# Kernel tuning notes

Hardware: AMD Instinct MI355X
Metric: run time of the kernel (lower is better)

The kernel has to match this reference:

```python
import jax, jax.numpy as jnp
import numpy as np

D_MODEL, D_K, D_V = 1024, 64, 64
B, S = 4, 2048

def setup_inputs() -> dict:
    key = jax.random.key(0)
    ks = jax.random.split(key, 9)
    lim = 1.0 / np.sqrt(D_MODEL)
    return {
        "query": jax.random.normal(ks[0], (B, S, D_MODEL), jnp.float32),
        "key":   jax.random.normal(ks[1], (B, S, D_MODEL), jnp.float32),
        "value": jax.random.normal(ks[2], (B, S, D_MODEL), jnp.float32),
        "Wq": jax.random.uniform(ks[3], (D_MODEL, D_K), jnp.float32, -lim, lim),
        "bq": jax.random.uniform(ks[4], (D_K,), jnp.float32, -lim, lim),
        "Wk": jax.random.uniform(ks[5], (D_MODEL, D_K), jnp.float32, -lim, lim),
        "bk": jax.random.uniform(ks[6], (D_K,), jnp.float32, -lim, lim),
        "Wv": jax.random.uniform(ks[7], (D_MODEL, D_V), jnp.float32, -lim, lim),
        "bv": jax.random.uniform(ks[8], (D_V,), jnp.float32, -lim, lim),
    }

def reference(query, key, value, Wq, bq, Wk, bk, Wv, bv):
    # Linear projections: [B,S,d_model] -> [B,S,d_k/d_v]
    q = jnp.einsum("bsd,dk->bsk", query, Wq) + bq
    k = jnp.einsum("bsd,dk->bsk", key, Wk) + bk
    v = jnp.einsum("bsd,dv->bsv", value, Wv) + bv
    scale = 1.0 / jnp.sqrt(jnp.asarray(q.shape[-1], q.dtype))
    scores = jnp.einsum("bqk,bsk->bqs", q, k) * scale  # [B,S,S]
    attn = jax.nn.softmax(scores, axis=-1)
    return jnp.einsum("bqs,bsv->bqv", attn, v)  # [B,S,d_v]
```

## Files before the change

kernel.cpp:

```cpp
#include <hip/hip_runtime.h>
#include <hip/hip_bf16.h>


typedef __attribute__((ext_vector_type(8))) short bf16x8;
typedef __attribute__((ext_vector_type(4))) float f32x4;

#define MFMA16(a, b, c) __builtin_amdgcn_mfma_f32_16x16x32_bf16((a), (b), (c), 0, 0, 0)

__device__ __forceinline__ unsigned short f2bf(float x) {
    unsigned int u = __float_as_uint(x);
    u = (u + 0x7FFFu + ((u >> 16) & 1u)) >> 16;
    return (unsigned short)u;
}

__global__ __launch_bounds__(256) void prep_w(
    const float* __restrict__ Wq, const float* __restrict__ Wk,
    const float* __restrict__ Wv, unsigned short* __restrict__ Wt) {
    int idx = blockIdx.x * 256 + threadIdx.x;
    int t = idx >> 16;
    int r = idx & 0xFFFF;
    int n = r >> 10, kk = r & 1023;
    const float* W = (t == 0) ? Wq : ((t == 1) ? Wk : Wv);
    Wt[idx] = f2bf(W[kk * 64 + n]);
}

__global__ __launch_bounds__(256) void proj_kernel(
    const float* __restrict__ xq, const float* __restrict__ xk,
    const float* __restrict__ xv, const unsigned short* __restrict__ Wt,
    const float* __restrict__ bq, const float* __restrict__ bk,
    const float* __restrict__ bv, unsigned short* __restrict__ outq,
    unsigned short* __restrict__ outk, unsigned short* __restrict__ outvt) {
    const int chunk = blockIdx.x;
    const int t = chunk >> 8;
    const int rb = chunk & 255;
    const int row0 = rb * 32;
    const float* __restrict__ x = (t == 0) ? xq : ((t == 1) ? xk : xv);
    const float* __restrict__ bias = (t == 0) ? bq : ((t == 1) ? bk : bv);
    const unsigned short* __restrict__ Wtt = Wt + t * 65536;

    __shared__ __align__(16) unsigned short xl[32][72];
    __shared__ __align__(16) unsigned short wl[64][72];

    const int tid = threadIdx.x;
    const int w = tid >> 6, l = tid & 63;
    const int lo = l & 15, q4 = l >> 4;
    const int rowt = (w & 1) * 16;
    const int colb = (w >> 1) * 32;

    const int lr = tid >> 3;
    const int lkc = (tid & 7) * 8;
    const int wr = tid >> 2;
    const int wkc = (tid & 3) * 16;

    f32x4 acc[2];
    for (int i = 0; i < 2; i++)
        for (int j = 0; j < 4; j++) acc[i][j] = 0.f;

    const float* xrow = x + (size_t)(row0 + lr) * 1024 + lkc;
    const unsigned short* wrow = Wtt + (size_t)wr * 1024 + wkc;

    float4 px0 = *(const float4*)(xrow);
    float4 px1 = *(const float4*)(xrow + 4);
    int4 pw0 = *(const int4*)(wrow);
    int4 pw1 = *(const int4*)(wrow + 8);

    for (int s = 0; s < 16; ++s) {
        __syncthreads();
        {
            int4 d;
            d.x = f2bf(px0.x) | ((int)f2bf(px0.y) << 16);
            d.y = f2bf(px0.z) | ((int)f2bf(px0.w) << 16);
            d.z = f2bf(px1.x) | ((int)f2bf(px1.y) << 16);
            d.w = f2bf(px1.z) | ((int)f2bf(px1.w) << 16);
            *(int4*)&xl[lr][lkc] = d;
            *(int4*)&wl[wr][wkc] = pw0;
            *(int4*)&wl[wr][wkc + 8] = pw1;
        }
        __syncthreads();
        if (s < 15) {
            const float* xn = xrow + (s + 1) * 64;
            px0 = *(const float4*)(xn);
            px1 = *(const float4*)(xn + 4);
            const unsigned short* wn = wrow + (s + 1) * 64;
            pw0 = *(const int4*)(wn);
            pw1 = *(const int4*)(wn + 8);
        }
        bf16x8 a0 = *(const bf16x8*)&xl[rowt + lo][q4 * 8];
        bf16x8 a1 = *(const bf16x8*)&xl[rowt + lo][32 + q4 * 8];
#pragma unroll
        for (int ci = 0; ci < 2; ++ci) {
            bf16x8 b0 = *(const bf16x8*)&wl[colb + ci * 16 + lo][q4 * 8];
            bf16x8 b1 = *(const bf16x8*)&wl[colb + ci * 16 + lo][32 + q4 * 8];
            acc[ci] = MFMA16(a0, b0, acc[ci]);
            acc[ci] = MFMA16(a1, b1, acc[ci]);
        }
    }
#pragma unroll
    for (int ci = 0; ci < 2; ++ci) {
        float bb = bias[colb + ci * 16 + lo];
#pragma unroll
        for (int i = 0; i < 4; i++) acc[ci][i] += bb;
    }
    if (t == 0) {
        const float SC = 0.125f * 1.44269504088896340736f;
#pragma unroll
        for (int ci = 0; ci < 2; ++ci)
#pragma unroll
            for (int i = 0; i < 4; i++) acc[ci][i] *= SC;
    }
    if (t < 2) {
        unsigned short* out = (t == 0) ? outq : outk;
#pragma unroll
        for (int ci = 0; ci < 2; ++ci)
#pragma unroll
            for (int i = 0; i < 4; i++)
                out[(size_t)(row0 + rowt + q4 * 4 + i) * 64 + colb + ci * 16 + lo] =
                    f2bf(acc[ci][i]);
    } else {
        int b = row0 >> 11;
        int sl = (row0 & 2047) + rowt + q4 * 4;
#pragma unroll
        for (int ci = 0; ci < 2; ++ci) {
            int vf = colb + ci * 16 + lo;
            ushort4 h;
            h.x = f2bf(acc[ci][0]);
            h.y = f2bf(acc[ci][1]);
            h.z = f2bf(acc[ci][2]);
            h.w = f2bf(acc[ci][3]);
            *(ushort4*)&outvt[(size_t)(b * 64 + vf) * 2048 + sl] = h;
        }
    }
}

__global__ __launch_bounds__(256) void flash_kernel(
    const unsigned short* __restrict__ q, const unsigned short* __restrict__ k,
    const unsigned short* __restrict__ vt, float* __restrict__ Opart,
    float* __restrict__ lpart) {
    const int bx = blockIdx.x;
    const int xcd = bx & 7;
    const int b = xcd >> 1;
    const int j = ((bx >> 3) << 1) | (xcd & 1);
    const int ks = j & 3;
    const int qb = j >> 2;
    const int w = threadIdx.x >> 6, l = threadIdx.x & 63;
    const int lo = l & 15, q4 = l >> 4;

    __shared__ __align__(16) unsigned short pl[4][16][72];

    const int srow = qb * 64 + w * 16;

    const unsigned short* qp = q + (size_t)(b * 2048 + srow + lo) * 64 + q4 * 8;
    bf16x8 aq0 = *(const bf16x8*)(qp);
    bf16x8 aq1 = *(const bf16x8*)(qp + 32);

    f32x4 O[4];
    for (int i = 0; i < 4; i++)
        for (int j2 = 0; j2 < 4; j2++) O[i][j2] = 0.f;
    float ll[4] = {0.f, 0.f, 0.f, 0.f};

    for (int kt = 0; kt < 8; ++kt) {
        const int kb = ks * 512 + kt * 64;
        f32x4 S[4];
        for (int i = 0; i < 4; i++)
            for (int j2 = 0; j2 < 4; j2++) S[i][j2] = 0.f;
        const unsigned short* kp = k + (size_t)(b * 2048 + kb + lo) * 64 + q4 * 8;
#pragma unroll
        for (int ct = 0; ct < 4; ++ct) {
            bf16x8 b0 = *(const bf16x8*)(kp + ct * 1024);
            bf16x8 b1 = *(const bf16x8*)(kp + ct * 1024 + 32);
            S[ct] = MFMA16(aq0, b0, S[ct]);
            S[ct] = MFMA16(aq1, b1, S[ct]);
        }
#pragma unroll
        for (int i = 0; i < 4; i++) {
#pragma unroll
            for (int ct = 0; ct < 4; ++ct) {
                float p = exp2f(S[ct][i]);
                S[ct][i] = p;
                ll[i] += p;
            }
#pragma unroll
            for (int ct = 0; ct < 4; ++ct)
                pl[w][q4 * 4 + i][ct * 16 + lo] = f2bf(S[ct][i]);
        }
        bf16x8 ap0 = *(const bf16x8*)&pl[w][lo][q4 * 8];
        bf16x8 ap1 = *(const bf16x8*)&pl[w][lo][32 + q4 * 8];
        const unsigned short* vp =
            vt + (size_t)(b * 64 + lo) * 2048 + kb + q4 * 8;
#pragma unroll
        for (int ct = 0; ct < 4; ++ct) {
            bf16x8 v0 = *(const bf16x8*)(vp + (size_t)ct * 16 * 2048);
            bf16x8 v1 = *(const bf16x8*)(vp + (size_t)ct * 16 * 2048 + 32);
            O[ct] = MFMA16(ap0, v0, O[ct]);
            O[ct] = MFMA16(ap1, v1, O[ct]);
        }
    }
    float* op = Opart + ((size_t)(b * 4 + ks) * 2048 + srow) * 64;
#pragma unroll
    for (int ct = 0; ct < 4; ++ct)
#pragma unroll
        for (int i = 0; i < 4; i++)
            op[(size_t)(q4 * 4 + i) * 64 + ct * 16 + lo] = O[ct][i];
#pragma unroll
    for (int i = 0; i < 4; i++) {
        float s = ll[i];
        s += __shfl_xor(s, 1);
        s += __shfl_xor(s, 2);
        s += __shfl_xor(s, 4);
        s += __shfl_xor(s, 8);
        if (lo == 0)
            lpart[(size_t)(b * 4 + ks) * 2048 + srow + q4 * 4 + i] = s;
    }
}

__global__ __launch_bounds__(256) void combine_kernel(
    const float* __restrict__ Opart, const float* __restrict__ lpart,
    float* __restrict__ out) {
    int idx = blockIdx.x * 256 + threadIdx.x;
    int rowi = idx >> 4;
    int v4 = (idx & 15) * 4;
    int b = rowi >> 11, s = rowi & 2047;
    float L = 0.f;
#pragma unroll
    for (int ks = 0; ks < 4; ++ks)
        L += lpart[(size_t)(b * 4 + ks) * 2048 + s];
    float inv = 1.f / L;
    float ax = 0.f, ay = 0.f, az = 0.f, aw = 0.f;
#pragma unroll
    for (int ks = 0; ks < 4; ++ks) {
        const float4 o =
            *(const float4*)&Opart[((size_t)(b * 4 + ks) * 2048 + s) * 64 + v4];
        ax += o.x;
        ay += o.y;
        az += o.z;
        aw += o.w;
    }
    float4 res = make_float4(ax * inv, ay * inv, az * inv, aw * inv);
    *(float4*)&out[(size_t)rowi * 64 + v4] = res;
}

extern "C" void kernel_launch(void* const* d_in, const int* in_sizes, int n_in,
                              void* d_out, int out_size, void* d_ws,
                              size_t ws_size, hipStream_t stream) {
    const float* xq = (const float*)d_in[0];
    const float* xk = (const float*)d_in[1];
    const float* xv = (const float*)d_in[2];
    const float* Wq = (const float*)d_in[3];
    const float* bq = (const float*)d_in[4];
    const float* Wk = (const float*)d_in[5];
    const float* bk = (const float*)d_in[6];
    const float* Wv = (const float*)d_in[7];
    const float* bv = (const float*)d_in[8];
    float* out = (float*)d_out;

    char* ws = (char*)d_ws;
    unsigned short* qb = (unsigned short*)(ws);
    unsigned short* kb = (unsigned short*)(ws + (1u << 20));
    unsigned short* vtb = (unsigned short*)(ws + (2u << 20));
    unsigned short* Wt = (unsigned short*)(ws + (3u << 20));
    float* Opart = (float*)(ws + 3538944);
    float* lpart = (float*)(ws + 11927552);

    hipLaunchKernelGGL(prep_w, dim3(768), dim3(256), 0, stream, Wq, Wk, Wv, Wt);
    hipLaunchKernelGGL(proj_kernel, dim3(768), dim3(256), 0, stream, xq, xk, xv,
                       Wt, bq, bk, bv, qb, kb, vtb);
    hipLaunchKernelGGL(flash_kernel, dim3(512), dim3(256), 0, stream, qb, kb,
                       vtb, Opart, lpart);
    hipLaunchKernelGGL(combine_kernel, dim3(512), dim3(256), 0, stream, Opart,
                       lpart, out);
}
```

Baseline: 174.4 us.

## Load projection operands directly into MFMA registers, dropping LDS staging

The projection kernel no longer stages x and W tiles through shared memory with barriers. Each wave now loads its fp32 x fragment and bf16 W fragment straight from global memory into MFMA operand registers, with a 16-row tile per block and twice as many blocks. This removes the LDS round-trips and __syncthreads overhead. In exchange, the four waves of a block each re-read the same x rows from global memory or cache, and the 16-byte-per-lane loads are strided by row, which may coalesce less well.

After: 211.7 us. +21.4%, slower.

```diff
diff --git a/kernel.cpp b/kernel.cpp
--- a/kernel.cpp
+++ b/kernel.cpp
@@ -31,104 +31,61 @@
     const float* __restrict__ bv, unsigned short* __restrict__ outq,
     unsigned short* __restrict__ outk, unsigned short* __restrict__ outvt) {
     const int chunk = blockIdx.x;
-    const int t = chunk >> 8;
-    const int rb = chunk & 255;
-    const int row0 = rb * 32;
+    const int t = chunk >> 9;
+    const int rb = chunk & 511;
+    const int row0 = rb * 16;
     const float* __restrict__ x = (t == 0) ? xq : ((t == 1) ? xk : xv);
     const float* __restrict__ bias = (t == 0) ? bq : ((t == 1) ? bk : bv);
-    const unsigned short* __restrict__ Wtt = Wt + t * 65536;
-
-    __shared__ __align__(16) unsigned short xl[32][72];
-    __shared__ __align__(16) unsigned short wl[64][72];
 
     const int tid = threadIdx.x;
     const int w = tid >> 6, l = tid & 63;
     const int lo = l & 15, q4 = l >> 4;
-    const int rowt = (w & 1) * 16;
-    const int colb = (w >> 1) * 32;
-
-    const int lr = tid >> 3;
-    const int lkc = (tid & 7) * 8;
-    const int wr = tid >> 2;
-    const int wkc = (tid & 3) * 16;
-
-    f32x4 acc[2];
-    for (int i = 0; i < 2; i++)
-        for (int j = 0; j < 4; j++) acc[i][j] = 0.f;
-
-    const float* xrow = x + (size_t)(row0 + lr) * 1024 + lkc;
-    const unsigned short* wrow = Wtt + (size_t)wr * 1024 + wkc;
-
-    float4 px0 = *(const float4*)(xrow);
-    float4 px1 = *(const float4*)(xrow + 4);
-    int4 pw0 = *(const int4*)(wrow);
-    int4 pw1 = *(const int4*)(wrow + 8);
-
-    for (int s = 0; s < 16; ++s) {
-        __syncthreads();
-        {
-            int4 d;
-            d.x = f2bf(px0.x) | ((int)f2bf(px0.y) << 16);
-            d.y = f2bf(px0.z) | ((int)f2bf(px0.w) << 16);
-            d.z = f2bf(px1.x) | ((int)f2bf(px1.y) << 16);
-            d.w = f2bf(px1.z) | ((int)f2bf(px1.w) << 16);
-            *(int4*)&xl[lr][lkc] = d;
-            *(int4*)&wl[wr][wkc] = pw0;
-            *(int4*)&wl[wr][wkc + 8] = pw1;
-        }
-        __syncthreads();
-        if (s < 15) {
-            const float* xn = xrow + (s + 1) * 64;
-            px0 = *(const float4*)(xn);
-            px1 = *(const float4*)(xn + 4);
-            const unsigned short* wn = wrow + (s + 1) * 64;
-            pw0 = *(const int4*)(wn);
-            pw1 = *(const int4*)(wn + 8);
-        }
-        bf16x8 a0 = *(const bf16x8*)&xl[rowt + lo][q4 * 8];
-        bf16x8 a1 = *(const bf16x8*)&xl[rowt + lo][32 + q4 * 8];
-#pragma unroll
-        for (int ci = 0; ci < 2; ++ci) {
-            bf16x8 b0 = *(const bf16x8*)&wl[colb + ci * 16 + lo][q4 * 8];
-            bf16x8 b1 = *(const bf16x8*)&wl[colb + ci * 16 + lo][32 + q4 * 8];
-            acc[ci] = MFMA16(a0, b0, acc[ci]);
-            acc[ci] = MFMA16(a1, b1, acc[ci]);
-        }
-    }
-#pragma unroll
-    for (int ci = 0; ci < 2; ++ci) {
-        float bb = bias[colb + ci * 16 + lo];
-#pragma unroll
-        for (int i = 0; i < 4; i++) acc[ci][i] += bb;
-    }
+
+    const float* __restrict__ xrow = x + (size_t)(row0 + lo) * 1024 + q4 * 8;
+    const unsigned short* __restrict__ wrow =
+        Wt + (size_t)t * 65536 + (size_t)(w * 16 + lo) * 1024 + q4 * 8;
+
+    f32x4 acc = {0.f, 0.f, 0.f, 0.f};
+#pragma unroll 8
+    for (int kk = 0; kk < 32; ++kk) {
+        float4 xa = *(const float4*)(xrow + kk * 32);
+        float4 xb = *(const float4*)(xrow + kk * 32 + 4);
+        bf16x8 bw = *(const bf16x8*)(wrow + kk * 32);
+        bf16x8 av;
+        av[0] = (short)f2bf(xa.x);
+        av[1] = (short)f2bf(xa.y);
+        av[2] = (short)f2bf(xa.z);
+        av[3] = (short)f2bf(xa.w);
+        av[4] = (short)f2bf(xb.x);
+        av[5] = (short)f2bf(xb.y);
+        av[6] = (short)f2bf(xb.z);
+        av[7] = (short)f2bf(xb.w);
+        acc = MFMA16(av, bw, acc);
+    }
+
+    float bb = bias[w * 16 + lo];
+#pragma unroll
+    for (int i = 0; i < 4; i++) acc[i] += bb;
     if (t == 0) {
         const float SC = 0.125f * 1.44269504088896340736f;
 #pragma unroll
-        for (int ci = 0; ci < 2; ++ci)
-#pragma unroll
-            for (int i = 0; i < 4; i++) acc[ci][i] *= SC;
+        for (int i = 0; i < 4; i++) acc[i] *= SC;
     }
     if (t < 2) {
         unsigned short* out = (t == 0) ? outq : outk;
 #pragma unroll
-        for (int ci = 0; ci < 2; ++ci)
-#pragma unroll
-            for (int i = 0; i < 4; i++)
-                out[(size_t)(row0 + rowt + q4 * 4 + i) * 64 + colb + ci * 16 + lo] =
-                    f2bf(acc[ci][i]);
+        for (int i = 0; i < 4; i++)
+            out[(size_t)(row0 + q4 * 4 + i) * 64 + w * 16 + lo] = f2bf(acc[i]);
     } else {
         int b = row0 >> 11;
-        int sl = (row0 & 2047) + rowt + q4 * 4;
-#pragma unroll
-        for (int ci = 0; ci < 2; ++ci) {
-            int vf = colb + ci * 16 + lo;
-            ushort4 h;
-            h.x = f2bf(acc[ci][0]);
-            h.y = f2bf(acc[ci][1]);
-            h.z = f2bf(acc[ci][2]);
-            h.w = f2bf(acc[ci][3]);
-            *(ushort4*)&outvt[(size_t)(b * 64 + vf) * 2048 + sl] = h;
-        }
+        int sl = (row0 & 2047) + q4 * 4;
+        int vf = w * 16 + lo;
+        ushort4 h;
+        h.x = f2bf(acc[0]);
+        h.y = f2bf(acc[1]);
+        h.z = f2bf(acc[2]);
+        h.w = f2bf(acc[3]);
+        *(ushort4*)&outvt[(size_t)(b * 64 + vf) * 2048 + sl] = h;
     }
 }
 
@@ -262,7 +219,7 @@
     float* lpart = (float*)(ws + 11927552);
 
     hipLaunchKernelGGL(prep_w, dim3(768), dim3(256), 0, stream, Wq, Wk, Wv, Wt);
-    hipLaunchKernelGGL(proj_kernel, dim3(768), dim3(256), 0, stream, xq, xk, xv,
+    hipLaunchKernelGGL(proj_kernel, dim3(1536), dim3(256), 0, stream, xq, xk, xv,
                        Wt, bq, bk, bv, qb, kb, vtb);
     hipLaunchKernelGGL(flash_kernel, dim3(512), dim3(256), 0, stream, qb, kb,
                        vtb, Opart, lpart);
```

## Double-buffer LDS tiles and prefetch two stages ahead in projection kernel

Applied to the files above, without the earlier changes.

The projection GEMM now uses two LDS buffers for the x and W tiles and keeps two register sets of global loads in flight. This cuts the per-iteration barriers from two to one and overlaps global loads and bf16 conversion with MFMA work. In exchange it uses twice the shared memory and more registers, which could lower occupancy. The projection is memory-bound on the fp32 input reads, so the gain depends on how much latency was exposed before.

New measurement: 176.6 us. Within noise of the previous version (+1.3%).

```diff
diff --git a/kernel.cpp b/kernel.cpp
--- a/kernel.cpp
+++ b/kernel.cpp
@@ -38,8 +38,8 @@
     const float* __restrict__ bias = (t == 0) ? bq : ((t == 1) ? bk : bv);
     const unsigned short* __restrict__ Wtt = Wt + t * 65536;
 
-    __shared__ __align__(16) unsigned short xl[32][72];
-    __shared__ __align__(16) unsigned short wl[64][72];
+    __shared__ __align__(16) unsigned short xl[2][32][72];
+    __shared__ __align__(16) unsigned short wl[2][64][72];
 
     const int tid = threadIdx.x;
     const int w = tid >> 6, l = tid & 63;
@@ -59,42 +59,67 @@
     const float* xrow = x + (size_t)(row0 + lr) * 1024 + lkc;
     const unsigned short* wrow = Wtt + (size_t)wr * 1024 + wkc;
 
-    float4 px0 = *(const float4*)(xrow);
-    float4 px1 = *(const float4*)(xrow + 4);
-    int4 pw0 = *(const int4*)(wrow);
-    int4 pw1 = *(const int4*)(wrow + 8);
-
-    for (int s = 0; s < 16; ++s) {
+    float4 pxA0, pxA1, pxB0, pxB1;
+    int4 pwA0, pwA1, pwB0, pwB1;
+
+#define LOADSET(X0, X1, W0, W1, s)                                            \
+    do {                                                                      \
+        const float* xn = xrow + (s) * 64;                                    \
+        X0 = *(const float4*)(xn);                                            \
+        X1 = *(const float4*)(xn + 4);                                        \
+        const unsigned short* wn = wrow + (s) * 64;                           \
+        W0 = *(const int4*)(wn);                                              \
+        W1 = *(const int4*)(wn + 8);                                          \
+    } while (0)
+
+#define WRITESET(X0, X1, W0, W1, bi)                                          \
+    do {                                                                      \
+        int4 d;                                                               \
+        d.x = f2bf(X0.x) | ((int)f2bf(X0.y) << 16);                           \
+        d.y = f2bf(X0.z) | ((int)f2bf(X0.w) << 16);                           \
+        d.z = f2bf(X1.x) | ((int)f2bf(X1.y) << 16);                           \
+        d.w = f2bf(X1.z) | ((int)f2bf(X1.w) << 16);                           \
+        *(int4*)&xl[bi][lr][lkc] = d;                                         \
+        *(int4*)&wl[bi][wr][wkc] = W0;                                        \
+        *(int4*)&wl[bi][wr][wkc + 8] = W1;                                    \
+    } while (0)
+
+#define COMPUTE(bi)                                                           \
+    do {                                                                      \
+        bf16x8 a0 = *(const bf16x8*)&xl[bi][rowt + lo][q4 * 8];               \
+        bf16x8 a1 = *(const bf16x8*)&xl[bi][rowt + lo][32 + q4 * 8];          \
+        _Pragma("unroll")                                                     \
+        for (int ci = 0; ci < 2; ++ci) {                                      \
+            bf16x8 b0 = *(const bf16x8*)&wl[bi][colb + ci * 16 + lo][q4 * 8]; \
+            bf16x8 b1 =                                                       \
+                *(const bf16x8*)&wl[bi][colb + ci * 16 + lo][32 + q4 * 8];    \
+            acc[ci] = MFMA16(a0, b0, acc[ci]);                                \
+            acc[ci] = MFMA16(a1, b1, acc[ci]);                                \
+        }                                                                     \
+    } while (0)
+
+    LOADSET(pxA0, pxA1, pwA0, pwA1, 0);
+    WRITESET(pxA0, pxA1, pwA0, pwA1, 0);
+    LOADSET(pxB0, pxB1, pwB0, pwB1, 1);
+    LOADSET(pxA0, pxA1, pwA0, pwA1, 2);
+    __syncthreads();
+
+#pragma unroll
+    for (int ss = 0; ss < 8; ++ss) {
+        const int s = ss * 2;
+        if (s < 15) WRITESET(pxB0, pxB1, pwB0, pwB1, 1);
+        if (s < 13) LOADSET(pxB0, pxB1, pwB0, pwB1, s + 3);
+        COMPUTE(0);
         __syncthreads();
-        {
-            int4 d;
-            d.x = f2bf(px0.x) | ((int)f2bf(px0.y) << 16);
-            d.y = f2bf(px0.z) | ((int)f2bf(px0.w) << 16);
-            d.z = f2bf(px1.x) | ((int)f2bf(px1.y) << 16);
-            d.w = f2bf(px1.z) | ((int)f2bf(px1.w) << 16);
-            *(int4*)&xl[lr][lkc] = d;
-            *(int4*)&wl[wr][wkc] = pw0;
-            *(int4*)&wl[wr][wkc + 8] = pw1;
-        }
+        if (s + 1 < 15) WRITESET(pxA0, pxA1, pwA0, pwA1, 0);
+        if (s + 1 < 13) LOADSET(pxA0, pxA1, pwA0, pwA1, s + 4);
+        COMPUTE(1);
         __syncthreads();
-        if (s < 15) {
-            const float* xn = xrow + (s + 1) * 64;
-            px0 = *(const float4*)(xn);
-            px1 = *(const float4*)(xn + 4);
-            const unsigned short* wn = wrow + (s + 1) * 64;
-            pw0 = *(const int4*)(wn);
-            pw1 = *(const int4*)(wn + 8);
-        }
-        bf16x8 a0 = *(const bf16x8*)&xl[rowt + lo][q4 * 8];
-        bf16x8 a1 = *(const bf16x8*)&xl[rowt + lo][32 + q4 * 8];
-#pragma unroll
-        for (int ci = 0; ci < 2; ++ci) {
-            bf16x8 b0 = *(const bf16x8*)&wl[colb + ci * 16 + lo][q4 * 8];
-            bf16x8 b1 = *(const bf16x8*)&wl[colb + ci * 16 + lo][32 + q4 * 8];
-            acc[ci] = MFMA16(a0, b0, acc[ci]);
-            acc[ci] = MFMA16(a1, b1, acc[ci]);
-        }
-    }
+    }
+#undef LOADSET
+#undef WRITESET
+#undef COMPUTE
+
 #pragma unroll
     for (int ci = 0; ci < 2; ++ci) {
         float bb = bias[colb + ci * 16 + lo];
```

## Pipeline projection loads via direct-to-LDS async copies and double the flash key splits

Applied to the files above, without the earlier changes.

The projection kernel now stages fp32 activation and bf16 weight tiles straight into double-buffered, XOR-swizzled shared memory with global_load_lds. It converts to bf16 at fragment-read time, so the next tile's loads overlap the current MFMAs instead of passing through registers. The flash kernel splits the key dimension 8 ways instead of 4 and launches 1024 blocks, for more parallelism on the 256-CU device. The cost is twice the partial output and sum traffic in the combine step, plus a larger workspace.

New measurement: 175.8 us. Within noise of the previous version (+0.8%).

```diff
diff --git a/kernel.cpp b/kernel.cpp
--- a/kernel.cpp
+++ b/kernel.cpp
@@ -11,6 +11,24 @@
     unsigned int u = __float_as_uint(x);
     u = (u + 0x7FFFu + ((u >> 16) & 1u)) >> 16;
     return (unsigned short)u;
+}
+
+typedef __attribute__((address_space(1))) const void* gas1_t;
+typedef __attribute__((address_space(3))) void* las3_t;
+__device__ __forceinline__ void glds16(const void* g, void* l) {
+    __builtin_amdgcn_global_load_lds((gas1_t)g, (las3_t)l, 16, 0, 0);
+}
+
+#define WAITV(N) asm volatile("s_waitcnt vmcnt(" #N ")" ::: "memory")
+#define FENCE() __builtin_amdgcn_sched_barrier(0)
+
+__device__ __forceinline__ bf16x8 cvt8(f32x4 a, f32x4 b) {
+    bf16x8 r;
+    r[0] = (short)f2bf(a[0]); r[1] = (short)f2bf(a[1]);
+    r[2] = (short)f2bf(a[2]); r[3] = (short)f2bf(a[3]);
+    r[4] = (short)f2bf(b[0]); r[5] = (short)f2bf(b[1]);
+    r[6] = (short)f2bf(b[2]); r[7] = (short)f2bf(b[3]);
+    return r;
 }
 
 __global__ __launch_bounds__(256) void prep_w(
@@ -38,8 +56,8 @@
     const float* __restrict__ bias = (t == 0) ? bq : ((t == 1) ? bk : bv);
     const unsigned short* __restrict__ Wtt = Wt + t * 65536;
 
-    __shared__ __align__(16) unsigned short xl[32][72];
-    __shared__ __align__(16) unsigned short wl[64][72];
+    __shared__ __align__(16) float xs[2][2048];
+    __shared__ __align__(16) unsigned short wsb[2][4096];
 
     const int tid = threadIdx.x;
     const int w = tid >> 6, l = tid & 63;
@@ -47,54 +65,70 @@
     const int rowt = (w & 1) * 16;
     const int colb = (w >> 1) * 32;
 
-    const int lr = tid >> 3;
-    const int lkc = (tid & 7) * 8;
-    const int wr = tid >> 2;
-    const int wkc = (tid & 3) * 16;
+    const int xr0 = tid >> 4;
+    const int xgp = ((tid & 15) ^ (xr0 & 7)) * 4;
+    const float* xg0 = x + (size_t)(row0 + xr0) * 1024 + xgp;
+    const float* xg1 = x + (size_t)(row0 + 16 + xr0) * 1024 + xgp;
+    const int wr0 = tid >> 3;
+    const int wgp = ((tid & 7) ^ (wr0 & 7)) * 8;
+    const unsigned short* wg0 = Wtt + (size_t)wr0 * 1024 + wgp;
+    const unsigned short* wg1 = Wtt + (size_t)(32 + wr0) * 1024 + wgp;
+
+#define STAGE(bi, s)                                                          \
+    do {                                                                      \
+        glds16(xg0 + (s) * 64, &xs[bi][w * 256]);                             \
+        glds16(xg1 + (s) * 64, &xs[bi][1024 + w * 256]);                      \
+        glds16(wg0 + (s) * 64, &wsb[bi][w * 512]);                            \
+        glds16(wg1 + (s) * 64, &wsb[bi][2048 + w * 512]);                     \
+    } while (0)
 
     f32x4 acc[2];
     for (int i = 0; i < 2; i++)
         for (int j = 0; j < 4; j++) acc[i][j] = 0.f;
 
-    const float* xrow = x + (size_t)(row0 + lr) * 1024 + lkc;
-    const unsigned short* wrow = Wtt + (size_t)wr * 1024 + wkc;
-
-    float4 px0 = *(const float4*)(xrow);
-    float4 px1 = *(const float4*)(xrow + 4);
-    int4 pw0 = *(const int4*)(wrow);
-    int4 pw1 = *(const int4*)(wrow + 8);
-
+#define COMPUTE(bi)                                                           \
+    do {                                                                      \
+        const int Ra = rowt + lo;                                             \
+        const int ax = (Ra & 7) << 4;                                         \
+        const char* xb = (const char*)&xs[bi][0] + Ra * 256;                  \
+        f32x4 va0 = *(const f32x4*)(xb + ((q4 * 32) ^ ax));                   \
+        f32x4 va1 = *(const f32x4*)(xb + ((q4 * 32 + 16) ^ ax));              \
+        f32x4 va2 = *(const f32x4*)(xb + ((128 + q4 * 32) ^ ax));             \
+        f32x4 va3 = *(const f32x4*)(xb + ((128 + q4 * 32 + 16) ^ ax));        \
+        bf16x8 a0 = cvt8(va0, va1);                                           \
+        bf16x8 a1 = cvt8(va2, va3);                                           \
+        _Pragma("unroll")                                                     \
+        for (int ci = 0; ci < 2; ++ci) {                                      \
+            const int Rb = colb + ci * 16 + lo;                               \
+            const int bx2 = (Rb & 7) << 4;                                    \
+            const char* wb2 = (const char*)&wsb[bi][0] + Rb * 128;            \
+            bf16x8 b0 = *(const bf16x8*)(wb2 + ((q4 * 16) ^ bx2));            \
+            bf16x8 b1 = *(const bf16x8*)(wb2 + ((64 + q4 * 16) ^ bx2));       \
+            acc[ci] = MFMA16(a0, b0, acc[ci]);                                \
+            acc[ci] = MFMA16(a1, b1, acc[ci]);                                \
+        }                                                                     \
+    } while (0)
+
+    STAGE(0, 0);
+    STAGE(1, 1);
+
+#pragma unroll
     for (int s = 0; s < 16; ++s) {
-        __syncthreads();
-        {
-            int4 d;
-            d.x = f2bf(px0.x) | ((int)f2bf(px0.y) << 16);
-            d.y = f2bf(px0.z) | ((int)f2bf(px0.w) << 16);
-            d.z = f2bf(px1.x) | ((int)f2bf(px1.y) << 16);
-            d.w = f2bf(px1.z) | ((int)f2bf(px1.w) << 16);
-            *(int4*)&xl[lr][lkc] = d;
-            *(int4*)&wl[wr][wkc] = pw0;
-            *(int4*)&wl[wr][wkc + 8] = pw1;
-        }
-        __syncthreads();
-        if (s < 15) {
-            const float* xn = xrow + (s + 1) * 64;
-            px0 = *(const float4*)(xn);
-            px1 = *(const float4*)(xn + 4);
-            const unsigned short* wn = wrow + (s + 1) * 64;
-            pw0 = *(const int4*)(wn);
-            pw1 = *(const int4*)(wn + 8);
-        }
-        bf16x8 a0 = *(const bf16x8*)&xl[rowt + lo][q4 * 8];
-        bf16x8 a1 = *(const bf16x8*)&xl[rowt + lo][32 + q4 * 8];
-#pragma unroll
-        for (int ci = 0; ci < 2; ++ci) {
-            bf16x8 b0 = *(const bf16x8*)&wl[colb + ci * 16 + lo][q4 * 8];
-            bf16x8 b1 = *(const bf16x8*)&wl[colb + ci * 16 + lo][32 + q4 * 8];
-            acc[ci] = MFMA16(a0, b0, acc[ci]);
-            acc[ci] = MFMA16(a1, b1, acc[ci]);
-        }
-    }
+        if (s < 15) { WAITV(4); } else { WAITV(0); }
+        FENCE();
+        __builtin_amdgcn_s_barrier();
+        FENCE();
+        if (s & 1) COMPUTE(1); else COMPUTE(0);
+        FENCE();
+        __builtin_amdgcn_s_barrier();
+        FENCE();
+        if (s + 2 < 16) {
+            if (s & 1) STAGE(1, s + 2); else STAGE(0, s + 2);
+        }
+    }
+#undef STAGE
+#undef COMPUTE
+
 #pragma unroll
     for (int ci = 0; ci < 2; ++ci) {
         float bb = bias[colb + ci * 16 + lo];
@@ -140,8 +174,8 @@
     const int xcd = bx & 7;
     const int b = xcd >> 1;
     const int j = ((bx >> 3) << 1) | (xcd & 1);
-    const int ks = j & 3;
-    const int qb = j >> 2;
+    const int ks = j & 7;
+    const int qb = j >> 3;
     const int w = threadIdx.x >> 6, l = threadIdx.x & 63;
     const int lo = l & 15, q4 = l >> 4;
 
@@ -158,8 +192,8 @@
         for (int j2 = 0; j2 < 4; j2++) O[i][j2] = 0.f;
     float ll[4] = {0.f, 0.f, 0.f, 0.f};
 
-    for (int kt = 0; kt < 8; ++kt) {
-        const int kb = ks * 512 + kt * 64;
+    for (int kt = 0; kt < 4; ++kt) {
+        const int kb = ks * 256 + kt * 64;
         f32x4 S[4];
         for (int i = 0; i < 4; i++)
             for (int j2 = 0; j2 < 4; j2++) S[i][j2] = 0.f;
@@ -195,7 +229,7 @@
             O[ct] = MFMA16(ap1, v1, O[ct]);
         }
     }
-    float* op = Opart + ((size_t)(b * 4 + ks) * 2048 + srow) * 64;
+    float* op = Opart + ((size_t)(b * 8 + ks) * 2048 + srow) * 64;
 #pragma unroll
     for (int ct = 0; ct < 4; ++ct)
 #pragma unroll
@@ -209,7 +243,7 @@
         s += __shfl_xor(s, 4);
         s += __shfl_xor(s, 8);
         if (lo == 0)
-            lpart[(size_t)(b * 4 + ks) * 2048 + srow + q4 * 4 + i] = s;
+            lpart[(size_t)(b * 8 + ks) * 2048 + srow + q4 * 4 + i] = s;
     }
 }
 
@@ -222,14 +256,14 @@
     int b = rowi >> 11, s = rowi & 2047;
     float L = 0.f;
 #pragma unroll
-    for (int ks = 0; ks < 4; ++ks)
-        L += lpart[(size_t)(b * 4 + ks) * 2048 + s];
+    for (int ks = 0; ks < 8; ++ks)
+        L += lpart[(size_t)(b * 8 + ks) * 2048 + s];
     float inv = 1.f / L;
     float ax = 0.f, ay = 0.f, az = 0.f, aw = 0.f;
 #pragma unroll
-    for (int ks = 0; ks < 4; ++ks) {
+    for (int ks = 0; ks < 8; ++ks) {
         const float4 o =
-            *(const float4*)&Opart[((size_t)(b * 4 + ks) * 2048 + s) * 64 + v4];
+            *(const float4*)&Opart[((size_t)(b * 8 + ks) * 2048 + s) * 64 + v4];
         ax += o.x;
         ay += o.y;
         az += o.z;
@@ -258,13 +292,13 @@
     unsigned short* kb = (unsigned short*)(ws + (1u << 20));
     unsigned short* vtb = (unsigned short*)(ws + (2u << 20));
     unsigned short* Wt = (unsigned short*)(ws + (3u << 20));
-    float* Opart = (float*)(ws + 3538944);
-    float* lpart = (float*)(ws + 11927552);
+    float* Opart = (float*)(ws + (4u << 20));
+    float* lpart = (float*)(ws + (20u << 20));
 
     hipLaunchKernelGGL(prep_w, dim3(768), dim3(256), 0, stream, Wq, Wk, Wv, Wt);
     hipLaunchKernelGGL(proj_kernel, dim3(768), dim3(256), 0, stream, xq, xk, xv,
                        Wt, bq, bk, bv, qb, kb, vtb);
-    hipLaunchKernelGGL(flash_kernel, dim3(512), dim3(256), 0, stream, qb, kb,
+    hipLaunchKernelGGL(flash_kernel, dim3(1024), dim3(256), 0, stream, qb, kb,
                        vtb, Opart, lpart);
     hipLaunchKernelGGL(combine_kernel, dim3(512), dim3(256), 0, stream, Opart,
                        lpart, out);
```
